# Kernel tuning notes

Measured on AMD Instinct MI355X. Metric: run time of the kernel, lower is better.

Reference implementation:

```python
import jax, jax.numpy as jnp
import numpy as np

QBITS = 8  # all quant points configured to 8-bit symmetric by default


def fake_quant(v, bits=QBITS):
    """Symmetric per-tensor fake quantize/dequantize with STE-compatible form."""
    qmax = float(2 ** (bits - 1) - 1)
    scale = jnp.maximum(jnp.max(jnp.abs(v)) / qmax, 1e-8)
    q = jnp.clip(jnp.round(v / scale), -qmax - 1.0, qmax) * scale
    # straight-through estimator (identity gradient)
    return v + jax.lax.stop_gradient(q - v)


def reorder_pt_to_haste(w):
    # PyTorch gate order (r,z,n) -> Haste order (z,r,n) along leading 3H axis
    h3 = w.shape[0] // 3
    return jnp.concatenate([w[h3:2 * h3], w[:h3], w[2 * h3:]], axis=0)


def setup_inputs() -> dict:
    key = jax.random.key(0)
    ks = jax.random.split(key, 6)
    T, B, I, H = 1024, 64, 256, 256
    s = 1.0 / np.sqrt(H)
    return {
        "x": jax.random.normal(ks[0], (T, B, I), dtype=jnp.float32),
        "weight_ih": jax.random.normal(ks[1], (3 * H, I), dtype=jnp.float32) * s,
        "weight_hh": jax.random.normal(ks[2], (3 * H, H), dtype=jnp.float32) * s,
        "bias_ih": jax.random.normal(ks[3], (3 * H,), dtype=jnp.float32) * s,
        "bias_hh": jax.random.normal(ks[4], (3 * H,), dtype=jnp.float32) * s,
        "h0": jax.random.normal(ks[5], (B, H), dtype=jnp.float32),
    }


def _quant_gru(x, weight_ih, weight_hh, bias_ih, bias_hh, h0):
    T, B, I = x.shape
    H = weight_hh.shape[1]
    # Haste layout: W [I,3H], R [H,3H], gate order (z,r,n)
    W = reorder_pt_to_haste(weight_ih).T   # [I, 3H]
    R = reorder_pt_to_haste(weight_hh).T   # [H, 3H]
    bx = reorder_pt_to_haste(bias_ih)      # [3H]
    br = reorder_pt_to_haste(bias_hh)      # [3H]

    # per-tensor fake quant of inputs / weights / biases
    xq = fake_quant(x)
    Wq = fake_quant(W)
    Rq = fake_quant(R)
    bxq = fake_quant(bx)
    brq = fake_quant(br)

    # precompute Wx for all timesteps: [T,B,3H], quantized matmul output
    Wx = fake_quant(jnp.einsum('tbi,ih->tbh', xq, Wq))

    bx_z, bx_r, bx_n = bxq[:H], bxq[H:2 * H], bxq[2 * H:]
    br_z, br_r, br_n = brq[:H], brq[H:2 * H], brq[2 * H:]

    def step(h, wx_t):
        hq = fake_quant(h)
        Rh = fake_quant(hq @ Rq)           # [B, 3H]
        Rh_z, Rh_r, Rh_n = Rh[:, :H], Rh[:, H:2 * H], Rh[:, 2 * H:]
        wx_z, wx_r, wx_n = wx_t[:, :H], wx_t[:, H:2 * H], wx_t[:, 2 * H:]

        z_pre = fake_quant(wx_z + bx_z + Rh_z + br_z)
        z = fake_quant(jax.nn.sigmoid(z_pre))
        r_pre = fake_quant(wx_r + bx_r + Rh_r + br_r)
        r = fake_quant(jax.nn.sigmoid(r_pre))

        Rh_add_br = fake_quant(Rh_n + br_n)
        rRh = fake_quant(r * Rh_add_br)
        g_pre = fake_quant(wx_n + bx_n + rRh)
        g = fake_quant(jnp.tanh(g_pre))

        old_contrib = fake_quant(z * h)
        new_contrib = fake_quant((1.0 - z) * g)
        h_new = old_contrib + new_contrib
        return h_new, h_new

    h_last, output = jax.lax.scan(step, h0, Wx)  # output: [T, B, H]
    return output, h_last[None]  # h_n: [1, B, H]


def reference(x, weight_ih, weight_hh, bias_ih, bias_hh, h0):
    return _quant_gru(x, weight_ih, weight_hh, bias_ih, bias_hh, h0)
```

## Files before the change

### kernel.cpp

```cpp
#include <hip/hip_runtime.h>
#include <cstdint>
#include <cstddef>


typedef int   v4i __attribute__((ext_vector_type(4)));
typedef float v4f __attribute__((ext_vector_type(4)));

#define T_STEPS 1024
#define OUT_MAIN_FLOATS (1024*64*256)
#define WXQ_DOUT_OFF 16842752

__device__ __forceinline__ float clamp128(float x) {
  return fminf(fmaxf(x, -128.0f), 127.0f);
}
__device__ __forceinline__ int permj(int j) {
  return j < 256 ? j + 256 : (j < 512 ? j - 256 : j);
}
__device__ __forceinline__ float sigmoidf_(float x) {
  return __fdividef(1.0f, 1.0f + __expf(-x));
}
__device__ __forceinline__ float tanhf_(float x) {
  float e = __expf(-2.0f * fabsf(x));
  float t = __fdividef(1.0f - e, 1.0f + e);
  return copysignf(t, x);
}
__device__ __forceinline__ unsigned skey(float x) {
  unsigned u = __float_as_uint(x);
  return (u & 0x80000000u) ? ~u : (u | 0x80000000u);
}
__device__ __forceinline__ float sdec(unsigned k) {
  unsigned u = (k & 0x80000000u) ? (k ^ 0x80000000u) : ~k;
  return __uint_as_float(u);
}
__device__ __forceinline__ float wave_amax(float v) {
  #pragma unroll
  for (int m = 1; m <= 32; m <<= 1) v = fmaxf(v, __shfl_xor(v, m, 64));
  return v;
}

#define MFMA_I8(a, b, c) __builtin_amdgcn_mfma_i32_16x16x64_i8(a, b, c, 0, 0, 0)

__global__ void k_absmax(const float* __restrict__ p, int n4, unsigned* slot) {
  int i = blockIdx.x * blockDim.x + threadIdx.x;
  int stride = gridDim.x * blockDim.x;
  const v4f* p4 = (const v4f*)p;
  float m = 0.0f;
  for (; i < n4; i += stride) {
    v4f v = p4[i];
    m = fmaxf(m, fmaxf(fmaxf(fabsf(v[0]), fabsf(v[1])),
                       fmaxf(fabsf(v[2]), fabsf(v[3]))));
  }
  m = wave_amax(m);
  if ((threadIdx.x & 63) == 0) atomicMax(slot, __float_as_uint(m));
}

__global__ void k_frag(const float* __restrict__ src,
                       const unsigned* __restrict__ slots, int slot_idx,
                       signed char* __restrict__ dst) {
  int id = blockIdx.x * 256 + threadIdx.x;
  float s = fmaxf(__uint_as_float(slots[slot_idx]) / 127.0f, 1e-8f);
  int bq   = id & 3;
  int lane = (id >> 2) & 63;
  int kc   = (id >> 8) & 3;
  int ct   = id >> 10;
  int n = ct * 16 + (lane & 15);
  int k = kc * 64 + (lane >> 4) * 16 + bq * 4;
  const float* p = src + permj(n) * 256 + k;
  int b0 = ((int)clamp128(rintf(p[0] / s))) & 255;
  int b1 = ((int)clamp128(rintf(p[1] / s))) & 255;
  int b2 = ((int)clamp128(rintf(p[2] / s))) & 255;
  int b3 = ((int)clamp128(rintf(p[3] / s))) & 255;
  ((int*)dst)[id] = b0 | (b1 << 8) | (b2 << 16) | (b3 << 24);
}

__global__ void k_bias(const float* __restrict__ bih, const float* __restrict__ bhh,
                       const unsigned* __restrict__ slots, float* __restrict__ bqo) {
  int j = threadIdx.x;
  float s_bx = fmaxf(__uint_as_float(slots[3]) / 127.0f, 1e-8f);
  float s_br = fmaxf(__uint_as_float(slots[4]) / 127.0f, 1e-8f);
  int pr = permj(j);
  bqo[j]       = s_bx * clamp128(rintf(bih[pr] / s_bx));
  bqo[768 + j] = s_br * clamp128(rintf(bhh[pr] / s_br));
}

__global__ void k_xq(const float* __restrict__ x, const unsigned* __restrict__ slots,
                     signed char* __restrict__ xq8, int n4) {
  int i = blockIdx.x * blockDim.x + threadIdx.x;
  if (i >= n4) return;
  float s_x = fmaxf(__uint_as_float(slots[0]) / 127.0f, 1e-8f);
  v4f v = ((const v4f*)x)[i];
  int b0 = ((int)clamp128(rintf(v[0] / s_x))) & 255;
  int b1 = ((int)clamp128(rintf(v[1] / s_x))) & 255;
  int b2 = ((int)clamp128(rintf(v[2] / s_x))) & 255;
  int b3 = ((int)clamp128(rintf(v[3] / s_x))) & 255;
  ((int*)xq8)[i] = b0 | (b1 << 8) | (b2 << 16) | (b3 << 24);
}

__global__ __launch_bounds__(1024) void k_wx_i8(
    const signed char* __restrict__ xq8, const signed char* __restrict__ wf,
    unsigned* __restrict__ slots, signed char* __restrict__ wxq, int mode) {
  const int t = blockIdx.x;
  const int tid = threadIdx.x, lane = tid & 63, w = tid >> 6;
  const int cl = lane & 15, lh = lane >> 4;

  v4i Bz[4], Br[4], Bn[4];
  #pragma unroll
  for (int kc = 0; kc < 4; ++kc) {
    Bz[kc] = *(const v4i*)(wf + (((w)*4      + kc) * 64 + lane) * 16);
    Br[kc] = *(const v4i*)(wf + (((w + 16)*4 + kc) * 64 + lane) * 16);
    Bn[kc] = *(const v4i*)(wf + (((w + 32)*4 + kc) * 64 + lane) * 16);
  }
  v4i acc[3][4];
  #pragma unroll
  for (int p = 0; p < 3; ++p)
    #pragma unroll
    for (int rt = 0; rt < 4; ++rt) acc[p][rt] = (v4i){0, 0, 0, 0};

  const signed char* xr = xq8 + t * 16384;
  #pragma unroll
  for (int kc = 0; kc < 4; ++kc)
    #pragma unroll
    for (int rt = 0; rt < 4; ++rt) {
      v4i A = *(const v4i*)(xr + (rt * 16 + cl) * 256 + kc * 64 + lh * 16);
      acc[0][rt] = MFMA_I8(A, Bz[kc], acc[0][rt]);
      acc[1][rt] = MFMA_I8(A, Br[kc], acc[1][rt]);
      acc[2][rt] = MFMA_I8(A, Bn[kc], acc[2][rt]);
    }

  if (mode == 0) {
    int mm = 0;
    #pragma unroll
    for (int p = 0; p < 3; ++p)
      #pragma unroll
      for (int rt = 0; rt < 4; ++rt)
        #pragma unroll
        for (int rg = 0; rg < 4; ++rg) mm = max(mm, abs(acc[p][rt][rg]));
    #pragma unroll
    for (int m = 1; m <= 32; m <<= 1) mm = max(mm, __shfl_xor(mm, m, 64));
    if (lane == 0) atomicMax((int*)(slots + 5), mm);
  } else {
    int islot = *(const int*)(slots + 5);
    float maxMf = (float)islot;
    float s_x = fmaxf(__uint_as_float(slots[0]) / 127.0f, 1e-8f);
    float s_W = fmaxf(__uint_as_float(slots[1]) / 127.0f, 1e-8f);
    float s_xW = s_x * s_W;
    float s_wx = fmaxf(s_xW * maxMf / 127.0f, 1e-8f);
    #pragma unroll
    for (int p = 0; p < 3; ++p)
      #pragma unroll
      for (int rt = 0; rt < 4; ++rt) {
        int dw = 0;
        #pragma unroll
        for (int rg = 0; rg < 4; ++rg) {
          float qf = clamp128(rintf((s_xW * (float)acc[p][rt][rg]) / s_wx));
          dw |= (((int)qf) & 255) << (rg * 8);
        }
        ((int*)wxq)[t * 12288 + p * 4096 + rt * 1024 + w * 64 + lh * 16 + cl] = dw;
      }
  }
}

template <int NCH>
__device__ __forceinline__ void xchg(unsigned* keys, unsigned tag,
    unsigned (*lred)[8], unsigned long long* gslot, int wg, int tid, int lane) {
  const int rset = tag % 3;
  #pragma unroll
  for (int c = 0; c < NCH; ++c) {
    unsigned v = keys[c];
    #pragma unroll
    for (int m = 1; m <= 32; m <<= 1)
      v = max(v, (unsigned)__shfl_xor((int)v, m, 64));
    keys[c] = v;
  }
  if (lane == 0) {
    #pragma unroll
    for (int c = 0; c < NCH; ++c) atomicMax(&lred[rset][c], keys[c]);
  }
  __syncthreads();
  const int par = tag & 1;
  if (tid < NCH) {
    unsigned long long v =
        ((unsigned long long)tag << 32) | (unsigned long long)lred[rset][tid];
    __hip_atomic_store(&gslot[(par * 4 + wg) * 8 + tid], v,
                       __ATOMIC_RELAXED, __HIP_MEMORY_SCOPE_AGENT);
  } else if (tid == 32) {
    int ns = rset + 1; if (ns == 3) ns = 0;
    #pragma unroll
    for (int c = 0; c < 8; ++c) lred[ns][c] = 0u;
  } else if (tid >= 64 && tid < 64 + 3 * NCH) {
    int idx = tid - 64;
    int owi = idx / NCH;
    int c = idx - owi * NCH;
    int ow = owi + (owi >= wg ? 1 : 0);
    unsigned long long* p = &gslot[(par * 4 + ow) * 8 + c];
    unsigned long long v;
    do {
      v = __hip_atomic_load(p, __ATOMIC_RELAXED, __HIP_MEMORY_SCOPE_AGENT);
    } while ((unsigned)(v >> 32) != tag);
    atomicMax(&lred[rset][c], (unsigned)v);
  }
  __syncthreads();
  #pragma unroll
  for (int c = 0; c < NCH; ++c) keys[c] = lred[rset][c];
}

__global__ __launch_bounds__(1024) void k_recur4b(
    const signed char* __restrict__ wxq, const signed char* __restrict__ brf,
    const float* __restrict__ bq, const unsigned* __restrict__ slots,
    const float* __restrict__ h0p, float* __restrict__ out,
    unsigned long long* __restrict__ gslot) {
  __shared__ signed char ah[16 * 272];
  __shared__ unsigned lred[3][8];

  const int tid = threadIdx.x;
  const int lane = tid & 63;
  const int w = tid >> 6;
  const int cl = lane & 15;
  const int lh = lane >> 4;
  const int wg = blockIdx.x;
  const int j = w * 16 + cl;
  const int brow = wg * 16 + lh * 4;

  if (tid < 24) ((unsigned*)lred)[tid] = 0u;

  float s_x = fmaxf(__uint_as_float(slots[0]) / 127.0f, 1e-8f);
  float s_W = fmaxf(__uint_as_float(slots[1]) / 127.0f, 1e-8f);
  float s_R = fmaxf(__uint_as_float(slots[2]) / 127.0f, 1e-8f);
  float maxM0 = (float)(*(const int*)(slots + 5));
  float s_wx = fmaxf(s_x * s_W * maxM0 / 127.0f, 1e-8f);

  float bxz = bq[j], bxr = bq[j + 256], bxn = bq[j + 512];
  float brz = bq[768 + j], brr = bq[1024 + j], brn = bq[1280 + j];

  v4i Bz[4], Br[4], Bn[4];
  #pragma unroll
  for (int kc = 0; kc < 4; ++kc) {
    Bz[kc] = *(const v4i*)(brf + (((w)*4      + kc) * 64 + lane) * 16);
    Br[kc] = *(const v4i*)(brf + (((w + 16)*4 + kc) * 64 + lane) * 16);
    Bn[kc] = *(const v4i*)(brf + (((w + 32)*4 + kc) * 64 + lane) * 16);
  }

  float h[4];
  #pragma unroll
  for (int rg = 0; rg < 4; ++rg) h[rg] = h0p[(brow + rg) * 256 + j];

  __syncthreads();

  unsigned tag = 1;
  float sh;
  {
    float m = fmaxf(fmaxf(fabsf(h[0]), fabsf(h[1])),
                    fmaxf(fabsf(h[2]), fabsf(h[3])));
    unsigned kk[1] = {__float_as_uint(m)};
    xchg<1>(kk, tag++, lred, gslot, wg, tid, lane);
    sh = fmaxf(__uint_as_float(kk[0]) / 127.0f, 1e-8f);
    float ish = 1.0f / sh;
    #pragma unroll
    for (int rg = 0; rg < 4; ++rg)
      ah[(lh * 4 + rg) * 272 + j] = (signed char)(int)rintf(h[rg] * ish);
    __syncthreads();
  }

  for (int t = 0; t < T_STEPS; ++t) {
    const signed char* wb = wxq + (size_t)t * 49152 + (wg << 12) + (tid << 2);
    int wvz = *(const int*)(wb);
    int wvr = *(const int*)(wb + 16384);
    int wvn = *(const int*)(wb + 32768);

    v4i az4 = {0,0,0,0}, ar4 = {0,0,0,0}, an4 = {0,0,0,0};
    #pragma unroll
    for (int kc = 0; kc < 4; ++kc) {
      v4i A = *(const v4i*)(ah + cl * 272 + kc * 64 + lh * 16);
      az4 = MFMA_I8(A, Bz[kc], az4);
      ar4 = MFMA_I8(A, Br[kc], ar4);
      an4 = MFMA_I8(A, Bn[kc], an4);
    }

    int mm = 0;
    #pragma unroll
    for (int rg = 0; rg < 4; ++rg)
      mm = max(mm, max(abs(az4[rg]), max(abs(ar4[rg]), abs(an4[rg]))));
    unsigned kk[5];
    kk[0] = (unsigned)mm;
    xchg<1>(kk, tag++, lred, gslot, wg, tid, lane);
    float maxMf = (float)(int)kk[0];
    float s_Rh = fmaxf(sh * s_R * maxMf / 127.0f, 1e-8f);
    float fRh = (sh * s_R) / s_Rh;

    float zp[4], rp[4], nb[4];
    float az = 0.0f, ar = 0.0f, an = 0.0f;
    float mzs = -3.402823466e38f, mrs = -3.402823466e38f;
    #pragma unroll
    for (int rg = 0; rg < 4; ++rg) {
      float Rz = s_Rh * rintf((float)az4[rg] * fRh);
      float Rr = s_Rh * rintf((float)ar4[rg] * fRh);
      float Rn = s_Rh * rintf((float)an4[rg] * fRh);
      float wz = s_wx * (float)((signed char)(wvz >> (rg * 8)));
      float wr = s_wx * (float)((signed char)(wvr >> (rg * 8)));
      float a1 = ((wz + bxz) + Rz) + brz;
      float a2 = ((wr + bxr) + Rr) + brr;
      float a3 = Rn + brn;
      zp[rg] = a1; rp[rg] = a2; nb[rg] = a3;
      az = fmaxf(az, fabsf(a1)); ar = fmaxf(ar, fabsf(a2));
      an = fmaxf(an, fabsf(a3));
      mzs = fmaxf(mzs, a1); mrs = fmaxf(mrs, a2);
    }
    kk[0] = __float_as_uint(az); kk[1] = __float_as_uint(ar);
    kk[2] = __float_as_uint(an); kk[3] = skey(mzs); kk[4] = skey(mrs);
    xchg<5>(kk, tag++, lred, gslot, wg, tid, lane);
    float s1 = fmaxf(__uint_as_float(kk[0]) / 127.0f, 1e-8f), i1 = 1.0f / s1;
    float s2 = fmaxf(__uint_as_float(kk[1]) / 127.0f, 1e-8f), i2 = 1.0f / s2;
    float s3 = fmaxf(__uint_as_float(kk[2]) / 127.0f, 1e-8f), i3 = 1.0f / s3;
    float zq_max = s1 * rintf(sdec(kk[3]) * i1);
    float rq_max = s2 * rintf(sdec(kk[4]) * i2);
    float s4 = fmaxf(sigmoidf_(zq_max) / 127.0f, 1e-8f), i4 = 1.0f / s4;
    float s5 = fmaxf(sigmoidf_(rq_max) / 127.0f, 1e-8f), i5 = 1.0f / s5;

    float zf[4], rr_[4];
    float m6 = 0.0f;
    #pragma unroll
    for (int rg = 0; rg < 4; ++rg) {
      float zq = s1 * rintf(zp[rg] * i1);
      float rq = s2 * rintf(rp[rg] * i2);
      float zv = sigmoidf_(zq);
      float rv = sigmoidf_(rq);
      zf[rg] = s4 * rintf(zv * i4);
      float rq2 = s5 * rintf(rv * i5);
      float nbq = s3 * rintf(nb[rg] * i3);
      float rr = rq2 * nbq;
      rr_[rg] = rr;
      m6 = fmaxf(m6, fabsf(rr));
    }
    kk[0] = __float_as_uint(m6);
    xchg<1>(kk, tag++, lred, gslot, wg, tid, lane);
    float s6 = fmaxf(__uint_as_float(kk[0]) / 127.0f, 1e-8f), i6 = 1.0f / s6;

    float gp[4];
    float m7 = 0.0f;
    #pragma unroll
    for (int rg = 0; rg < 4; ++rg) {
      float rrq = s6 * rintf(rr_[rg] * i6);
      float wn = s_wx * (float)((signed char)(wvn >> (rg * 8)));
      float g = (wn + bxn) + rrq;
      gp[rg] = g;
      m7 = fmaxf(m7, fabsf(g));
    }
    kk[0] = __float_as_uint(m7);
    xchg<1>(kk, tag++, lred, gslot, wg, tid, lane);
    float m7g = __uint_as_float(kk[0]);
    float s7 = fmaxf(m7g / 127.0f, 1e-8f), i7 = 1.0f / s7;
    float gq_max = s7 * rintf(m7g * i7);
    float s8 = fmaxf(tanhf_(gq_max) / 127.0f, 1e-8f), i8v = 1.0f / s8;

    float ov[4], nv[4];
    float mo = 0.0f, mn = 0.0f;
    #pragma unroll
    for (int rg = 0; rg < 4; ++rg) {
      float gpq = s7 * rintf(gp[rg] * i7);
      float gv = tanhf_(gpq);
      float gq = s8 * rintf(gv * i8v);
      float o = zf[rg] * h[rg];
      float n = (1.0f - zf[rg]) * gq;
      ov[rg] = o; nv[rg] = n;
      mo = fmaxf(mo, fabsf(o)); mn = fmaxf(mn, fabsf(n));
    }
    kk[0] = __float_as_uint(mo); kk[1] = __float_as_uint(mn);
    xchg<2>(kk, tag++, lred, gslot, wg, tid, lane);
    float s9  = fmaxf(__uint_as_float(kk[0]) / 127.0f, 1e-8f), i9  = 1.0f / s9;
    float s10 = fmaxf(__uint_as_float(kk[1]) / 127.0f, 1e-8f), i10 = 1.0f / s10;

    float mh = 0.0f;
    #pragma unroll
    for (int rg = 0; rg < 4; ++rg) {
      float oq = s9  * rintf(ov[rg] * i9);
      float nq = s10 * rintf(nv[rg] * i10);
      float hn = oq + nq;
      h[rg] = hn;
      mh = fmaxf(mh, fabsf(hn));
      out[t * 16384 + (brow + rg) * 256 + j] = hn;
    }
    kk[0] = __float_as_uint(mh);
    xchg<1>(kk, tag++, lred, gslot, wg, tid, lane);
    sh = fmaxf(__uint_as_float(kk[0]) / 127.0f, 1e-8f);
    float ish = 1.0f / sh;
    #pragma unroll
    for (int rg = 0; rg < 4; ++rg)
      ah[(lh * 4 + rg) * 272 + j] = (signed char)(int)rintf(h[rg] * ish);
    __syncthreads();
  }

  #pragma unroll
  for (int rg = 0; rg < 4; ++rg)
    out[OUT_MAIN_FLOATS + (brow + rg) * 256 + j] = h[rg];
}

extern "C" void kernel_launch(void* const* d_in, const int* in_sizes, int n_in,
                              void* d_out, int out_size, void* d_ws, size_t ws_size,
                              hipStream_t stream) {
  const float* x   = (const float*)d_in[0];
  const float* wih = (const float*)d_in[1];
  const float* whh = (const float*)d_in[2];
  const float* bih = (const float*)d_in[3];
  const float* bhh = (const float*)d_in[4];
  const float* h0  = (const float*)d_in[5];
  float* out = (float*)d_out;

  unsigned* slots = (unsigned*)d_ws;
  unsigned long long* gslot = (unsigned long long*)((char*)d_ws + 512);
  float* bq       = (float*)((char*)d_ws + 4096);
  signed char* F  = (signed char*)d_ws + 10240;

  signed char* wxq = (signed char*)d_out + WXQ_DOUT_OFF;
  signed char* xq8 = (signed char*)d_out;

  hipMemsetAsync(d_ws, 0, 4096, stream);

  k_absmax<<<dim3(1024), dim3(256), 0, stream>>>(x,   16777216 / 4, slots + 0);
  k_absmax<<<dim3(96),   dim3(256), 0, stream>>>(wih, 196608 / 4,   slots + 1);
  k_absmax<<<dim3(96),   dim3(256), 0, stream>>>(whh, 196608 / 4,   slots + 2);
  k_absmax<<<dim3(1),    dim3(256), 0, stream>>>(bih, 768 / 4,      slots + 3);
  k_absmax<<<dim3(1),    dim3(256), 0, stream>>>(bhh, 768 / 4,      slots + 4);

  k_frag<<<dim3(192), dim3(256), 0, stream>>>(wih, slots, 1, F);
  k_bias<<<dim3(1), dim3(768), 0, stream>>>(bih, bhh, slots, bq);
  k_xq<<<dim3(16384), dim3(256), 0, stream>>>(x, slots, xq8, 4194304);

  k_wx_i8<<<dim3(1024), dim3(1024), 0, stream>>>(xq8, F, slots, wxq, 0);
  k_wx_i8<<<dim3(1024), dim3(1024), 0, stream>>>(xq8, F, slots, wxq, 1);

  k_frag<<<dim3(192), dim3(256), 0, stream>>>(whh, slots, 2, F);

  k_recur4b<<<dim3(4), dim3(1024), 0, stream>>>(wxq, F, bq, slots, h0, out,
                                                gslot);
}
```

Baseline: 14.14 ms.

## Co-locate recurrence workgroups on one XCD and use cache-scoped flag exchange

Launches 256 workgroups and lets each block read its XCC id from a hardware register. The first XCC to gather four blocks is elected, and only those four run the recurrence; the other blocks exit. The cross-workgroup max exchange now writes flags with both sc0 and sc1 stores and polls mainly through the sc0 path, with an occasional sc1 load as a fallback. The intent is to keep the per-step inter-block synchronization inside one XCD's L2 and cut flag latency. In exchange it relies on undocumented cache-scope semantics and on enough blocks being co-resident on one XCD.

Measured after the change: 15.09 ms. +6.7%, slower.

```diff
diff --git a/kernel.cpp b/kernel.cpp
--- a/kernel.cpp
+++ b/kernel.cpp
@@ -35,6 +35,28 @@
 __device__ __forceinline__ float wave_amax(float v) {
   #pragma unroll
   for (int m = 1; m <= 32; m <<= 1) v = fmaxf(v, __shfl_xor(v, m, 64));
+  return v;
+}
+
+__device__ __forceinline__ void st_ab_u64(unsigned long long* pa,
+                                          unsigned long long* pb,
+                                          unsigned long long v) {
+  asm volatile("global_store_dwordx2 %0, %2, off sc0\n\t"
+               "global_store_dwordx2 %1, %2, off sc1"
+               :: "v"(pa), "v"(pb), "v"(v) : "memory");
+}
+__device__ __forceinline__ unsigned long long ld_a_u64(
+    const unsigned long long* p) {
+  unsigned long long v;
+  asm volatile("global_load_dwordx2 %0, %1, off sc0\n\ts_waitcnt vmcnt(0)"
+               : "=&v"(v) : "v"(p) : "memory");
+  return v;
+}
+__device__ __forceinline__ unsigned long long ld_b_u64(
+    const unsigned long long* p) {
+  unsigned long long v;
+  asm volatile("global_load_dwordx2 %0, %1, off sc1\n\ts_waitcnt vmcnt(0)"
+               : "=&v"(v) : "v"(p) : "memory");
   return v;
 }
 
@@ -162,7 +184,8 @@
 
 template <int NCH>
 __device__ __forceinline__ void xchg(unsigned* keys, unsigned tag,
-    unsigned (*lred)[8], unsigned long long* gslot, int wg, int tid, int lane) {
+    unsigned (*lred)[8], unsigned long long* gslotA, unsigned long long* gslotB,
+    int wg, int tid, int lane) {
   const int rset = tag % 3;
   #pragma unroll
   for (int c = 0; c < NCH; ++c) {
@@ -181,8 +204,8 @@
   if (tid < NCH) {
     unsigned long long v =
         ((unsigned long long)tag << 32) | (unsigned long long)lred[rset][tid];
-    __hip_atomic_store(&gslot[(par * 4 + wg) * 8 + tid], v,
-                       __ATOMIC_RELAXED, __HIP_MEMORY_SCOPE_AGENT);
+    int si = (par * 4 + wg) * 8 + tid;
+    st_ab_u64(&gslotA[si], &gslotB[si], v);
   } else if (tid == 32) {
     int ns = rset + 1; if (ns == 3) ns = 0;
     #pragma unroll
@@ -192,11 +215,19 @@
     int owi = idx / NCH;
     int c = idx - owi * NCH;
     int ow = owi + (owi >= wg ? 1 : 0);
-    unsigned long long* p = &gslot[(par * 4 + ow) * 8 + c];
+    int si = (par * 4 + ow) * 8 + c;
+    unsigned long long* pa = &gslotA[si];
+    unsigned long long* pb = &gslotB[si];
     unsigned long long v;
-    do {
-      v = __hip_atomic_load(p, __ATOMIC_RELAXED, __HIP_MEMORY_SCOPE_AGENT);
-    } while ((unsigned)(v >> 32) != tag);
+    int it = 0;
+    for (;;) {
+      v = ld_a_u64(pa);
+      if ((unsigned)(v >> 32) == tag) break;
+      if ((it++ & 3) == 3) {
+        v = ld_b_u64(pb);
+        if ((unsigned)(v >> 32) == tag) break;
+      }
+    }
     atomicMax(&lred[rset][c], (unsigned)v);
   }
   __syncthreads();
@@ -208,16 +239,37 @@
     const signed char* __restrict__ wxq, const signed char* __restrict__ brf,
     const float* __restrict__ bq, const unsigned* __restrict__ slots,
     const float* __restrict__ h0p, float* __restrict__ out,
-    unsigned long long* __restrict__ gslot) {
+    unsigned long long* __restrict__ gslotA,
+    unsigned long long* __restrict__ gslotB, int* ectl) {
   __shared__ signed char ah[16 * 272];
   __shared__ unsigned lred[3][8];
+  __shared__ int s_role;
 
   const int tid = threadIdx.x;
+
+  if (tid == 0) {
+    unsigned xcc = ((unsigned)__builtin_amdgcn_s_getreg(63508)) & 7u;
+    int role = -1;
+    int claim = atomicAdd(&ectl[xcc], 1);
+    if (claim < 4) {
+      if (claim == 3) atomicCAS(&ectl[8], 0, (int)xcc + 1);
+      int wv;
+      do {
+        wv = __hip_atomic_load(&ectl[8], __ATOMIC_RELAXED,
+                               __HIP_MEMORY_SCOPE_AGENT);
+      } while (wv == 0);
+      if (wv == (int)xcc + 1) role = claim;
+    }
+    s_role = role;
+  }
+  __syncthreads();
+  if (s_role < 0) return;
+  const int wg = s_role;
+
   const int lane = tid & 63;
   const int w = tid >> 6;
   const int cl = lane & 15;
   const int lh = lane >> 4;
-  const int wg = blockIdx.x;
   const int j = w * 16 + cl;
   const int brow = wg * 16 + lh * 4;
 
@@ -252,7 +304,7 @@
     float m = fmaxf(fmaxf(fabsf(h[0]), fabsf(h[1])),
                     fmaxf(fabsf(h[2]), fabsf(h[3])));
     unsigned kk[1] = {__float_as_uint(m)};
-    xchg<1>(kk, tag++, lred, gslot, wg, tid, lane);
+    xchg<1>(kk, tag++, lred, gslotA, gslotB, wg, tid, lane);
     sh = fmaxf(__uint_as_float(kk[0]) / 127.0f, 1e-8f);
     float ish = 1.0f / sh;
     #pragma unroll
@@ -282,7 +334,7 @@
       mm = max(mm, max(abs(az4[rg]), max(abs(ar4[rg]), abs(an4[rg]))));
     unsigned kk[5];
     kk[0] = (unsigned)mm;
-    xchg<1>(kk, tag++, lred, gslot, wg, tid, lane);
+    xchg<1>(kk, tag++, lred, gslotA, gslotB, wg, tid, lane);
     float maxMf = (float)(int)kk[0];
     float s_Rh = fmaxf(sh * s_R * maxMf / 127.0f, 1e-8f);
     float fRh = (sh * s_R) / s_Rh;
@@ -307,7 +359,7 @@
     }
     kk[0] = __float_as_uint(az); kk[1] = __float_as_uint(ar);
     kk[2] = __float_as_uint(an); kk[3] = skey(mzs); kk[4] = skey(mrs);
-    xchg<5>(kk, tag++, lred, gslot, wg, tid, lane);
+    xchg<5>(kk, tag++, lred, gslotA, gslotB, wg, tid, lane);
     float s1 = fmaxf(__uint_as_float(kk[0]) / 127.0f, 1e-8f), i1 = 1.0f / s1;
     float s2 = fmaxf(__uint_as_float(kk[1]) / 127.0f, 1e-8f), i2 = 1.0f / s2;
     float s3 = fmaxf(__uint_as_float(kk[2]) / 127.0f, 1e-8f), i3 = 1.0f / s3;
@@ -332,7 +384,7 @@
       m6 = fmaxf(m6, fabsf(rr));
     }
     kk[0] = __float_as_uint(m6);
-    xchg<1>(kk, tag++, lred, gslot, wg, tid, lane);
+    xchg<1>(kk, tag++, lred, gslotA, gslotB, wg, tid, lane);
     float s6 = fmaxf(__uint_as_float(kk[0]) / 127.0f, 1e-8f), i6 = 1.0f / s6;
 
     float gp[4];
@@ -346,7 +398,7 @@
       m7 = fmaxf(m7, fabsf(g));
     }
     kk[0] = __float_as_uint(m7);
-    xchg<1>(kk, tag++, lred, gslot, wg, tid, lane);
+    xchg<1>(kk, tag++, lred, gslotA, gslotB, wg, tid, lane);
     float m7g = __uint_as_float(kk[0]);
     float s7 = fmaxf(m7g / 127.0f, 1e-8f), i7 = 1.0f / s7;
     float gq_max = s7 * rintf(m7g * i7);
@@ -365,7 +417,7 @@
       mo = fmaxf(mo, fabsf(o)); mn = fmaxf(mn, fabsf(n));
     }
     kk[0] = __float_as_uint(mo); kk[1] = __float_as_uint(mn);
-    xchg<2>(kk, tag++, lred, gslot, wg, tid, lane);
+    xchg<2>(kk, tag++, lred, gslotA, gslotB, wg, tid, lane);
     float s9  = fmaxf(__uint_as_float(kk[0]) / 127.0f, 1e-8f), i9  = 1.0f / s9;
     float s10 = fmaxf(__uint_as_float(kk[1]) / 127.0f, 1e-8f), i10 = 1.0f / s10;
 
@@ -380,7 +432,7 @@
       out[t * 16384 + (brow + rg) * 256 + j] = hn;
     }
     kk[0] = __float_as_uint(mh);
-    xchg<1>(kk, tag++, lred, gslot, wg, tid, lane);
+    xchg<1>(kk, tag++, lred, gslotA, gslotB, wg, tid, lane);
     sh = fmaxf(__uint_as_float(kk[0]) / 127.0f, 1e-8f);
     float ish = 1.0f / sh;
     #pragma unroll
@@ -406,7 +458,9 @@
   float* out = (float*)d_out;
 
   unsigned* slots = (unsigned*)d_ws;
-  unsigned long long* gslot = (unsigned long long*)((char*)d_ws + 512);
+  unsigned long long* gslotA = (unsigned long long*)((char*)d_ws + 512);
+  int* ectl       = (int*)((char*)d_ws + 1024);
+  unsigned long long* gslotB = (unsigned long long*)((char*)d_ws + 2048);
   float* bq       = (float*)((char*)d_ws + 4096);
   signed char* F  = (signed char*)d_ws + 10240;
 
@@ -430,6 +484,6 @@
 
   k_frag<<<dim3(192), dim3(256), 0, stream>>>(whh, slots, 2, F);
 
-  k_recur4b<<<dim3(4), dim3(1024), 0, stream>>>(wxq, F, bq, slots, h0, out,
-                                                gslot);
-}
+  k_recur4b<<<dim3(256), dim3(1024), 0, stream>>>(wxq, F, bq, slots, h0, out,
+                                                  gslotA, gslotB, ectl);
+}
```

## Run GRU recurrence in one workgroup, dropping cross-block atomic exchanges

Applied to the files above, without the earlier changes.

The recurrent kernel moves from 4 cooperating workgroups, which exchanged per-step absmax values through global atomics with spin-waits, to a single 1024-thread workgroup that handles all 64 batch rows using only LDS reductions. Each wave now computes 4 row tiles, so it does four times the MFMA and elementwise work. To save registers it packs intermediates as int8 and reloads the recurrent weight fragments from global memory every step instead of keeping them in registers. The aim is to remove the multiple global-sync round trips per timestep. The cost is serialising all the work onto one CU.

Result: slower. 31.52 ms (+122.8%).

```diff
diff --git a/kernel.cpp b/kernel.cpp
--- a/kernel.cpp
+++ b/kernel.cpp
@@ -36,6 +36,9 @@
   #pragma unroll
   for (int m = 1; m <= 32; m <<= 1) v = fmaxf(v, __shfl_xor(v, m, 64));
   return v;
+}
+__device__ __forceinline__ float sgnb(int dw, int rg) {
+  return (float)((signed char)(dw >> (rg * 8)));
 }
 
 #define MFMA_I8(a, b, c) __builtin_amdgcn_mfma_i32_16x16x64_i8(a, b, c, 0, 0, 0)
@@ -161,8 +164,8 @@
 }
 
 template <int NCH>
-__device__ __forceinline__ void xchg(unsigned* keys, unsigned tag,
-    unsigned (*lred)[8], unsigned long long* gslot, int wg, int tid, int lane) {
+__device__ __forceinline__ void bred(unsigned* keys, unsigned tag,
+                                     unsigned (*lred)[8], int tid, int lane) {
   const int rset = tag % 3;
   #pragma unroll
   for (int c = 0; c < NCH; ++c) {
@@ -175,41 +178,21 @@
   if (lane == 0) {
     #pragma unroll
     for (int c = 0; c < NCH; ++c) atomicMax(&lred[rset][c], keys[c]);
-  }
-  __syncthreads();
-  const int par = tag & 1;
-  if (tid < NCH) {
-    unsigned long long v =
-        ((unsigned long long)tag << 32) | (unsigned long long)lred[rset][tid];
-    __hip_atomic_store(&gslot[(par * 4 + wg) * 8 + tid], v,
-                       __ATOMIC_RELAXED, __HIP_MEMORY_SCOPE_AGENT);
   } else if (tid == 32) {
     int ns = rset + 1; if (ns == 3) ns = 0;
     #pragma unroll
     for (int c = 0; c < 8; ++c) lred[ns][c] = 0u;
-  } else if (tid >= 64 && tid < 64 + 3 * NCH) {
-    int idx = tid - 64;
-    int owi = idx / NCH;
-    int c = idx - owi * NCH;
-    int ow = owi + (owi >= wg ? 1 : 0);
-    unsigned long long* p = &gslot[(par * 4 + ow) * 8 + c];
-    unsigned long long v;
-    do {
-      v = __hip_atomic_load(p, __ATOMIC_RELAXED, __HIP_MEMORY_SCOPE_AGENT);
-    } while ((unsigned)(v >> 32) != tag);
-    atomicMax(&lred[rset][c], (unsigned)v);
   }
   __syncthreads();
   #pragma unroll
   for (int c = 0; c < NCH; ++c) keys[c] = lred[rset][c];
 }
 
-__global__ __launch_bounds__(1024) void k_recur4b(
+__global__ __launch_bounds__(1024) void k_recur1(
     const signed char* __restrict__ wxq, const signed char* __restrict__ brf,
     const float* __restrict__ bq, const unsigned* __restrict__ slots,
-    const float* __restrict__ h0p, float* __restrict__ out,
-    unsigned long long* __restrict__ gslot) {
-  __shared__ signed char ah[16 * 272];
+    const float* __restrict__ h0p, float* __restrict__ out) {
+  __shared__ signed char ah[64 * 272];
   __shared__ unsigned lred[3][8];
 
   const int tid = threadIdx.x;
@@ -217,9 +200,7 @@
   const int w = tid >> 6;
   const int cl = lane & 15;
   const int lh = lane >> 4;
-  const int wg = blockIdx.x;
   const int j = w * 16 + cl;
-  const int brow = wg * 16 + lh * 4;
 
   if (tid < 24) ((unsigned*)lred)[tid] = 0u;
 
@@ -232,82 +213,112 @@
   float bxz = bq[j], bxr = bq[j + 256], bxn = bq[j + 512];
   float brz = bq[768 + j], brr = bq[1024 + j], brn = bq[1280 + j];
 
-  v4i Bz[4], Br[4], Bn[4];
-  #pragma unroll
-  for (int kc = 0; kc < 4; ++kc) {
-    Bz[kc] = *(const v4i*)(brf + (((w)*4      + kc) * 64 + lane) * 16);
-    Br[kc] = *(const v4i*)(brf + (((w + 16)*4 + kc) * 64 + lane) * 16);
-    Bn[kc] = *(const v4i*)(brf + (((w + 32)*4 + kc) * 64 + lane) * 16);
-  }
-
-  float h[4];
-  #pragma unroll
-  for (int rg = 0; rg < 4; ++rg) h[rg] = h0p[(brow + rg) * 256 + j];
+  const signed char* pBz = brf + (((w)*4)      * 64 + lane) * 16;
+  const signed char* pBr = brf + (((w + 16)*4) * 64 + lane) * 16;
+  const signed char* pBn = brf + (((w + 32)*4) * 64 + lane) * 16;
+  const int abase = cl * 272 + lh * 16;
+
+  float h[4][4];
+  #pragma unroll
+  for (int rt = 0; rt < 4; ++rt)
+    #pragma unroll
+    for (int rg = 0; rg < 4; ++rg)
+      h[rt][rg] = h0p[(rt * 16 + lh * 4 + rg) * 256 + j];
 
   __syncthreads();
 
   unsigned tag = 1;
   float sh;
   {
-    float m = fmaxf(fmaxf(fabsf(h[0]), fabsf(h[1])),
-                    fmaxf(fabsf(h[2]), fabsf(h[3])));
+    float m = 0.0f;
+    #pragma unroll
+    for (int rt = 0; rt < 4; ++rt)
+      #pragma unroll
+      for (int rg = 0; rg < 4; ++rg) m = fmaxf(m, fabsf(h[rt][rg]));
     unsigned kk[1] = {__float_as_uint(m)};
-    xchg<1>(kk, tag++, lred, gslot, wg, tid, lane);
+    bred<1>(kk, tag++, lred, tid, lane);
     sh = fmaxf(__uint_as_float(kk[0]) / 127.0f, 1e-8f);
     float ish = 1.0f / sh;
     #pragma unroll
-    for (int rg = 0; rg < 4; ++rg)
-      ah[(lh * 4 + rg) * 272 + j] = (signed char)(int)rintf(h[rg] * ish);
+    for (int rt = 0; rt < 4; ++rt)
+      #pragma unroll
+      for (int rg = 0; rg < 4; ++rg)
+        ah[(rt * 16 + lh * 4 + rg) * 272 + j] =
+            (signed char)(int)rintf(h[rt][rg] * ish);
     __syncthreads();
   }
 
   for (int t = 0; t < T_STEPS; ++t) {
-    const signed char* wb = wxq + (size_t)t * 49152 + (wg << 12) + (tid << 2);
-    int wvz = *(const int*)(wb);
-    int wvr = *(const int*)(wb + 16384);
-    int wvn = *(const int*)(wb + 32768);
-
-    v4i az4 = {0,0,0,0}, ar4 = {0,0,0,0}, an4 = {0,0,0,0};
+    const signed char* wb = wxq + (size_t)t * 49152 + (tid << 2);
+    int wv[3][4];
+    #pragma unroll
+    for (int p = 0; p < 3; ++p)
+      #pragma unroll
+      for (int rt = 0; rt < 4; ++rt)
+        wv[p][rt] = *(const int*)(wb + p * 16384 + rt * 4096);
+
+    v4i accZ[4], accR[4], accN[4];
+    #pragma unroll
+    for (int rt = 0; rt < 4; ++rt) {
+      accZ[rt] = (v4i){0,0,0,0}; accR[rt] = (v4i){0,0,0,0};
+      accN[rt] = (v4i){0,0,0,0};
+    }
     #pragma unroll
     for (int kc = 0; kc < 4; ++kc) {
-      v4i A = *(const v4i*)(ah + cl * 272 + kc * 64 + lh * 16);
-      az4 = MFMA_I8(A, Bz[kc], az4);
-      ar4 = MFMA_I8(A, Br[kc], ar4);
-      an4 = MFMA_I8(A, Bn[kc], an4);
+      v4i Bz = *(const v4i*)(pBz + kc * 1024);
+      v4i Br = *(const v4i*)(pBr + kc * 1024);
+      v4i Bn = *(const v4i*)(pBn + kc * 1024);
+      #pragma unroll
+      for (int rt = 0; rt < 4; ++rt) {
+        v4i A = *(const v4i*)(ah + abase + rt * 4352 + kc * 64);
+        accZ[rt] = MFMA_I8(A, Bz, accZ[rt]);
+        accR[rt] = MFMA_I8(A, Br, accR[rt]);
+        accN[rt] = MFMA_I8(A, Bn, accN[rt]);
+      }
     }
 
     int mm = 0;
     #pragma unroll
-    for (int rg = 0; rg < 4; ++rg)
-      mm = max(mm, max(abs(az4[rg]), max(abs(ar4[rg]), abs(an4[rg]))));
+    for (int rt = 0; rt < 4; ++rt)
+      #pragma unroll
+      for (int rg = 0; rg < 4; ++rg)
+        mm = max(mm, max(abs(accZ[rt][rg]),
+                         max(abs(accR[rt][rg]), abs(accN[rt][rg]))));
     unsigned kk[5];
     kk[0] = (unsigned)mm;
-    xchg<1>(kk, tag++, lred, gslot, wg, tid, lane);
+    bred<1>(kk, tag++, lred, tid, lane);
     float maxMf = (float)(int)kk[0];
     float s_Rh = fmaxf(sh * s_R * maxMf / 127.0f, 1e-8f);
     float fRh = (sh * s_R) / s_Rh;
 
-    float zp[4], rp[4], nb[4];
+    int kzp[4], krp[4], knp[4];
     float az = 0.0f, ar = 0.0f, an = 0.0f;
     float mzs = -3.402823466e38f, mrs = -3.402823466e38f;
     #pragma unroll
-    for (int rg = 0; rg < 4; ++rg) {
-      float Rz = s_Rh * rintf((float)az4[rg] * fRh);
-      float Rr = s_Rh * rintf((float)ar4[rg] * fRh);
-      float Rn = s_Rh * rintf((float)an4[rg] * fRh);
-      float wz = s_wx * (float)((signed char)(wvz >> (rg * 8)));
-      float wr = s_wx * (float)((signed char)(wvr >> (rg * 8)));
-      float a1 = ((wz + bxz) + Rz) + brz;
-      float a2 = ((wr + bxr) + Rr) + brr;
-      float a3 = Rn + brn;
-      zp[rg] = a1; rp[rg] = a2; nb[rg] = a3;
-      az = fmaxf(az, fabsf(a1)); ar = fmaxf(ar, fabsf(a2));
-      an = fmaxf(an, fabsf(a3));
-      mzs = fmaxf(mzs, a1); mrs = fmaxf(mrs, a2);
+    for (int rt = 0; rt < 4; ++rt) {
+      int pz = 0, pr = 0, pn = 0;
+      #pragma unroll
+      for (int rg = 0; rg < 4; ++rg) {
+        float fz = rintf((float)accZ[rt][rg] * fRh);
+        float fr = rintf((float)accR[rt][rg] * fRh);
+        float fn = rintf((float)accN[rt][rg] * fRh);
+        pz |= (((int)fz) & 255) << (rg * 8);
+        pr |= (((int)fr) & 255) << (rg * 8);
+        pn |= (((int)fn) & 255) << (rg * 8);
+        float wz = s_wx * sgnb(wv[0][rt], rg);
+        float wr = s_wx * sgnb(wv[1][rt], rg);
+        float a1 = ((wz + bxz) + (s_Rh * fz)) + brz;
+        float a2 = ((wr + bxr) + (s_Rh * fr)) + brr;
+        float a3 = (s_Rh * fn) + brn;
+        az = fmaxf(az, fabsf(a1)); ar = fmaxf(ar, fabsf(a2));
+        an = fmaxf(an, fabsf(a3));
+        mzs = fmaxf(mzs, a1); mrs = fmaxf(mrs, a2);
+      }
+      kzp[rt] = pz; krp[rt] = pr; knp[rt] = pn;
     }
     kk[0] = __float_as_uint(az); kk[1] = __float_as_uint(ar);
     kk[2] = __float_as_uint(an); kk[3] = skey(mzs); kk[4] = skey(mrs);
-    xchg<5>(kk, tag++, lred, gslot, wg, tid, lane);
+    bred<5>(kk, tag++, lred, tid, lane);
     float s1 = fmaxf(__uint_as_float(kk[0]) / 127.0f, 1e-8f), i1 = 1.0f / s1;
     float s2 = fmaxf(__uint_as_float(kk[1]) / 127.0f, 1e-8f), i2 = 1.0f / s2;
     float s3 = fmaxf(__uint_as_float(kk[2]) / 127.0f, 1e-8f), i3 = 1.0f / s3;
@@ -316,82 +327,113 @@
     float s4 = fmaxf(sigmoidf_(zq_max) / 127.0f, 1e-8f), i4 = 1.0f / s4;
     float s5 = fmaxf(sigmoidf_(rq_max) / 127.0f, 1e-8f), i5 = 1.0f / s5;
 
-    float zf[4], rr_[4];
+    int kz2p[4], k2p[4], k3p[4];
     float m6 = 0.0f;
     #pragma unroll
-    for (int rg = 0; rg < 4; ++rg) {
-      float zq = s1 * rintf(zp[rg] * i1);
-      float rq = s2 * rintf(rp[rg] * i2);
-      float zv = sigmoidf_(zq);
-      float rv = sigmoidf_(rq);
-      zf[rg] = s4 * rintf(zv * i4);
-      float rq2 = s5 * rintf(rv * i5);
-      float nbq = s3 * rintf(nb[rg] * i3);
-      float rr = rq2 * nbq;
-      rr_[rg] = rr;
-      m6 = fmaxf(m6, fabsf(rr));
+    for (int rt = 0; rt < 4; ++rt) {
+      int pz2 = 0, p2 = 0, p3 = 0;
+      #pragma unroll
+      for (int rg = 0; rg < 4; ++rg) {
+        float wz = s_wx * sgnb(wv[0][rt], rg);
+        float zp = ((wz + bxz) + (s_Rh * sgnb(kzp[rt], rg))) + brz;
+        float wr = s_wx * sgnb(wv[1][rt], rg);
+        float rp = ((wr + bxr) + (s_Rh * sgnb(krp[rt], rg))) + brr;
+        float nb = (s_Rh * sgnb(knp[rt], rg)) + brn;
+        float zq = s1 * rintf(zp * i1);
+        float rq = s2 * rintf(rp * i2);
+        float zv = sigmoidf_(zq);
+        float rv = sigmoidf_(rq);
+        float fz2 = rintf(zv * i4);
+        float f2  = rintf(rv * i5);
+        float f3  = rintf(nb * i3);
+        pz2 |= (((int)fz2) & 255) << (rg * 8);
+        p2  |= (((int)f2)  & 255) << (rg * 8);
+        p3  |= (((int)f3)  & 255) << (rg * 8);
+        float rr = (s5 * f2) * (s3 * f3);
+        m6 = fmaxf(m6, fabsf(rr));
+      }
+      kz2p[rt] = pz2; k2p[rt] = p2; k3p[rt] = p3;
     }
     kk[0] = __float_as_uint(m6);
-    xchg<1>(kk, tag++, lred, gslot, wg, tid, lane);
+    bred<1>(kk, tag++, lred, tid, lane);
     float s6 = fmaxf(__uint_as_float(kk[0]) / 127.0f, 1e-8f), i6 = 1.0f / s6;
 
-    float gp[4];
+    float gp[4][4];
     float m7 = 0.0f;
     #pragma unroll
-    for (int rg = 0; rg < 4; ++rg) {
-      float rrq = s6 * rintf(rr_[rg] * i6);
-      float wn = s_wx * (float)((signed char)(wvn >> (rg * 8)));
-      float g = (wn + bxn) + rrq;
-      gp[rg] = g;
-      m7 = fmaxf(m7, fabsf(g));
-    }
+    for (int rt = 0; rt < 4; ++rt)
+      #pragma unroll
+      for (int rg = 0; rg < 4; ++rg) {
+        float rr = (s5 * sgnb(k2p[rt], rg)) * (s3 * sgnb(k3p[rt], rg));
+        float rrq = s6 * rintf(rr * i6);
+        float wn = s_wx * sgnb(wv[2][rt], rg);
+        float g = (wn + bxn) + rrq;
+        gp[rt][rg] = g;
+        m7 = fmaxf(m7, fabsf(g));
+      }
     kk[0] = __float_as_uint(m7);
-    xchg<1>(kk, tag++, lred, gslot, wg, tid, lane);
+    bred<1>(kk, tag++, lred, tid, lane);
     float m7g = __uint_as_float(kk[0]);
     float s7 = fmaxf(m7g / 127.0f, 1e-8f), i7 = 1.0f / s7;
     float gq_max = s7 * rintf(m7g * i7);
     float s8 = fmaxf(tanhf_(gq_max) / 127.0f, 1e-8f), i8v = 1.0f / s8;
 
-    float ov[4], nv[4];
+    int kgp_[4];
     float mo = 0.0f, mn = 0.0f;
     #pragma unroll
-    for (int rg = 0; rg < 4; ++rg) {
-      float gpq = s7 * rintf(gp[rg] * i7);
-      float gv = tanhf_(gpq);
-      float gq = s8 * rintf(gv * i8v);
-      float o = zf[rg] * h[rg];
-      float n = (1.0f - zf[rg]) * gq;
-      ov[rg] = o; nv[rg] = n;
-      mo = fmaxf(mo, fabsf(o)); mn = fmaxf(mn, fabsf(n));
+    for (int rt = 0; rt < 4; ++rt) {
+      int pg = 0;
+      #pragma unroll
+      for (int rg = 0; rg < 4; ++rg) {
+        float gpq = s7 * rintf(gp[rt][rg] * i7);
+        float gv = tanhf_(gpq);
+        float fg = rintf(gv * i8v);
+        pg |= (((int)fg) & 255) << (rg * 8);
+        float zf = s4 * sgnb(kz2p[rt], rg);
+        float o = zf * h[rt][rg];
+        float n = (1.0f - zf) * (s8 * fg);
+        mo = fmaxf(mo, fabsf(o)); mn = fmaxf(mn, fabsf(n));
+      }
+      kgp_[rt] = pg;
     }
     kk[0] = __float_as_uint(mo); kk[1] = __float_as_uint(mn);
-    xchg<2>(kk, tag++, lred, gslot, wg, tid, lane);
+    bred<2>(kk, tag++, lred, tid, lane);
     float s9  = fmaxf(__uint_as_float(kk[0]) / 127.0f, 1e-8f), i9  = 1.0f / s9;
     float s10 = fmaxf(__uint_as_float(kk[1]) / 127.0f, 1e-8f), i10 = 1.0f / s10;
 
     float mh = 0.0f;
     #pragma unroll
-    for (int rg = 0; rg < 4; ++rg) {
-      float oq = s9  * rintf(ov[rg] * i9);
-      float nq = s10 * rintf(nv[rg] * i10);
-      float hn = oq + nq;
-      h[rg] = hn;
-      mh = fmaxf(mh, fabsf(hn));
-      out[t * 16384 + (brow + rg) * 256 + j] = hn;
-    }
+    for (int rt = 0; rt < 4; ++rt)
+      #pragma unroll
+      for (int rg = 0; rg < 4; ++rg) {
+        float zf = s4 * sgnb(kz2p[rt], rg);
+        float o = zf * h[rt][rg];
+        float n = (1.0f - zf) * (s8 * sgnb(kgp_[rt], rg));
+        float oq = s9  * rintf(o * i9);
+        float nq = s10 * rintf(n * i10);
+        float hn = oq + nq;
+        h[rt][rg] = hn;
+        mh = fmaxf(mh, fabsf(hn));
+        out[t * 16384 + (rt * 16 + lh * 4 + rg) * 256 + j] = hn;
+      }
     kk[0] = __float_as_uint(mh);
-    xchg<1>(kk, tag++, lred, gslot, wg, tid, lane);
+    bred<1>(kk, tag++, lred, tid, lane);
     sh = fmaxf(__uint_as_float(kk[0]) / 127.0f, 1e-8f);
     float ish = 1.0f / sh;
     #pragma unroll
+    for (int rt = 0; rt < 4; ++rt)
+      #pragma unroll
+      for (int rg = 0; rg < 4; ++rg)
+        ah[(rt * 16 + lh * 4 + rg) * 272 + j] =
+            (signed char)(int)rintf(h[rt][rg] * ish);
+    __syncthreads();
+  }
+
+  #pragma unroll
+  for (int rt = 0; rt < 4; ++rt)
+    #pragma unroll
     for (int rg = 0; rg < 4; ++rg)
-      ah[(lh * 4 + rg) * 272 + j] = (signed char)(int)rintf(h[rg] * ish);
-    __syncthreads();
-  }
-
-  #pragma unroll
-  for (int rg = 0; rg < 4; ++rg)
-    out[OUT_MAIN_FLOATS + (brow + rg) * 256 + j] = h[rg];
+      out[OUT_MAIN_FLOATS + (rt * 16 + lh * 4 + rg) * 256 + j] = h[rt][rg];
 }
 
 extern "C" void kernel_launch(void* const* d_in, const int* in_sizes, int n_in,
@@ -406,7 +448,6 @@
   float* out = (float*)d_out;
 
   unsigned* slots = (unsigned*)d_ws;
-  unsigned long long* gslot = (unsigned long long*)((char*)d_ws + 512);
   float* bq       = (float*)((char*)d_ws + 4096);
   signed char* F  = (signed char*)d_ws + 10240;
 
@@ -430,6 +471,5 @@
 
   k_frag<<<dim3(192), dim3(256), 0, stream>>>(whh, slots, 2, F);
 
-  k_recur4b<<<dim3(4), dim3(1024), 0, stream>>>(wxq, F, bq, slots, h0, out,
-                                                gslot);
-}
+  k_recur1<<<dim3(1), dim3(1024), 0, stream>>>(wxq, F, bq, slots, h0, out);
+}
```

## Publish per-wavefront partial maxima globally to drop one block barrier per exchange

Applied to the files above, without the earlier changes.

Each wavefront now writes its own tagged partial maximum straight to global slots, instead of first merging into LDS and passing a __syncthreads before one thread publishes the block result. Remote blocks poll 16x more slots (one per wavefront per channel) and merge them into LDS, so each exchange has one block barrier instead of two. The cost is more global polling traffic and more polling threads, plus a larger zeroed workspace region with shifted offsets for bq and the fragment buffers.

Result: slower. 18.25 ms (+29.0%).

```diff
diff --git a/kernel.cpp b/kernel.cpp
--- a/kernel.cpp
+++ b/kernel.cpp
@@ -162,7 +162,8 @@
 
 template <int NCH>
 __device__ __forceinline__ void xchg(unsigned* keys, unsigned tag,
-    unsigned (*lred)[8], unsigned long long* gslot, int wg, int tid, int lane) {
+    unsigned (*lred)[8], unsigned long long* gslot, int wg, int tid, int lane,
+    int w) {
   const int rset = tag % 3;
   #pragma unroll
   for (int c = 0; c < NCH; ++c) {
@@ -172,32 +173,34 @@
       v = max(v, (unsigned)__shfl_xor((int)v, m, 64));
     keys[c] = v;
   }
-  if (lane == 0) {
-    #pragma unroll
-    for (int c = 0; c < NCH; ++c) atomicMax(&lred[rset][c], keys[c]);
-  }
-  __syncthreads();
   const int par = tag & 1;
-  if (tid < NCH) {
+  if (lane < NCH) {
+    unsigned kv = keys[0];
+    #pragma unroll
+    for (int c = 1; c < NCH; ++c) if (lane == c) kv = keys[c];
     unsigned long long v =
-        ((unsigned long long)tag << 32) | (unsigned long long)lred[rset][tid];
-    __hip_atomic_store(&gslot[(par * 4 + wg) * 8 + tid], v,
+        ((unsigned long long)tag << 32) | (unsigned long long)kv;
+    __hip_atomic_store(&gslot[((par * 4 + wg) * 16 + w) * 5 + lane], v,
                        __ATOMIC_RELAXED, __HIP_MEMORY_SCOPE_AGENT);
+    atomicMax(&lred[rset][lane], kv);
   } else if (tid == 32) {
     int ns = rset + 1; if (ns == 3) ns = 0;
     #pragma unroll
     for (int c = 0; c < 8; ++c) lred[ns][c] = 0u;
-  } else if (tid >= 64 && tid < 64 + 3 * NCH) {
+  }
+  if (tid >= 64 && tid < 64 + 3 * 16 * NCH) {
     int idx = tid - 64;
-    int owi = idx / NCH;
-    int c = idx - owi * NCH;
+    int owi = idx / (16 * NCH);
+    int rem = idx - owi * (16 * NCH);
+    int wv = rem / NCH;
+    int ch = rem - wv * NCH;
     int ow = owi + (owi >= wg ? 1 : 0);
-    unsigned long long* p = &gslot[(par * 4 + ow) * 8 + c];
+    unsigned long long* p = &gslot[((par * 4 + ow) * 16 + wv) * 5 + ch];
     unsigned long long v;
     do {
       v = __hip_atomic_load(p, __ATOMIC_RELAXED, __HIP_MEMORY_SCOPE_AGENT);
     } while ((unsigned)(v >> 32) != tag);
-    atomicMax(&lred[rset][c], (unsigned)v);
+    atomicMax(&lred[rset][ch], (unsigned)v);
   }
   __syncthreads();
   #pragma unroll
@@ -252,7 +255,7 @@
     float m = fmaxf(fmaxf(fabsf(h[0]), fabsf(h[1])),
                     fmaxf(fabsf(h[2]), fabsf(h[3])));
     unsigned kk[1] = {__float_as_uint(m)};
-    xchg<1>(kk, tag++, lred, gslot, wg, tid, lane);
+    xchg<1>(kk, tag++, lred, gslot, wg, tid, lane, w);
     sh = fmaxf(__uint_as_float(kk[0]) / 127.0f, 1e-8f);
     float ish = 1.0f / sh;
     #pragma unroll
@@ -282,7 +285,7 @@
       mm = max(mm, max(abs(az4[rg]), max(abs(ar4[rg]), abs(an4[rg]))));
     unsigned kk[5];
     kk[0] = (unsigned)mm;
-    xchg<1>(kk, tag++, lred, gslot, wg, tid, lane);
+    xchg<1>(kk, tag++, lred, gslot, wg, tid, lane, w);
     float maxMf = (float)(int)kk[0];
     float s_Rh = fmaxf(sh * s_R * maxMf / 127.0f, 1e-8f);
     float fRh = (sh * s_R) / s_Rh;
@@ -307,7 +310,7 @@
     }
     kk[0] = __float_as_uint(az); kk[1] = __float_as_uint(ar);
     kk[2] = __float_as_uint(an); kk[3] = skey(mzs); kk[4] = skey(mrs);
-    xchg<5>(kk, tag++, lred, gslot, wg, tid, lane);
+    xchg<5>(kk, tag++, lred, gslot, wg, tid, lane, w);
     float s1 = fmaxf(__uint_as_float(kk[0]) / 127.0f, 1e-8f), i1 = 1.0f / s1;
     float s2 = fmaxf(__uint_as_float(kk[1]) / 127.0f, 1e-8f), i2 = 1.0f / s2;
     float s3 = fmaxf(__uint_as_float(kk[2]) / 127.0f, 1e-8f), i3 = 1.0f / s3;
@@ -332,7 +335,7 @@
       m6 = fmaxf(m6, fabsf(rr));
     }
     kk[0] = __float_as_uint(m6);
-    xchg<1>(kk, tag++, lred, gslot, wg, tid, lane);
+    xchg<1>(kk, tag++, lred, gslot, wg, tid, lane, w);
     float s6 = fmaxf(__uint_as_float(kk[0]) / 127.0f, 1e-8f), i6 = 1.0f / s6;
 
     float gp[4];
@@ -346,7 +349,7 @@
       m7 = fmaxf(m7, fabsf(g));
     }
     kk[0] = __float_as_uint(m7);
-    xchg<1>(kk, tag++, lred, gslot, wg, tid, lane);
+    xchg<1>(kk, tag++, lred, gslot, wg, tid, lane, w);
     float m7g = __uint_as_float(kk[0]);
     float s7 = fmaxf(m7g / 127.0f, 1e-8f), i7 = 1.0f / s7;
     float gq_max = s7 * rintf(m7g * i7);
@@ -365,7 +368,7 @@
       mo = fmaxf(mo, fabsf(o)); mn = fmaxf(mn, fabsf(n));
     }
     kk[0] = __float_as_uint(mo); kk[1] = __float_as_uint(mn);
-    xchg<2>(kk, tag++, lred, gslot, wg, tid, lane);
+    xchg<2>(kk, tag++, lred, gslot, wg, tid, lane, w);
     float s9  = fmaxf(__uint_as_float(kk[0]) / 127.0f, 1e-8f), i9  = 1.0f / s9;
     float s10 = fmaxf(__uint_as_float(kk[1]) / 127.0f, 1e-8f), i10 = 1.0f / s10;
 
@@ -380,7 +383,7 @@
       out[t * 16384 + (brow + rg) * 256 + j] = hn;
     }
     kk[0] = __float_as_uint(mh);
-    xchg<1>(kk, tag++, lred, gslot, wg, tid, lane);
+    xchg<1>(kk, tag++, lred, gslot, wg, tid, lane, w);
     sh = fmaxf(__uint_as_float(kk[0]) / 127.0f, 1e-8f);
     float ish = 1.0f / sh;
     #pragma unroll
@@ -407,13 +410,13 @@
 
   unsigned* slots = (unsigned*)d_ws;
   unsigned long long* gslot = (unsigned long long*)((char*)d_ws + 512);
-  float* bq       = (float*)((char*)d_ws + 4096);
-  signed char* F  = (signed char*)d_ws + 10240;
+  float* bq       = (float*)((char*)d_ws + 6144);
+  signed char* F  = (signed char*)d_ws + 12288;
 
   signed char* wxq = (signed char*)d_out + WXQ_DOUT_OFF;
   signed char* xq8 = (signed char*)d_out;
 
-  hipMemsetAsync(d_ws, 0, 4096, stream);
+  hipMemsetAsync(d_ws, 0, 6144, stream);
 
   k_absmax<<<dim3(1024), dim3(256), 0, stream>>>(x,   16777216 / 4, slots + 0);
   k_absmax<<<dim3(96),   dim3(256), 0, stream>>>(wih, 196608 / 4,   slots + 1);
```
